# Optimization experiments

Hardware: AMD Instinct MI355X
Metric: run time of the kernel (lower is better)

Reference implementation:

```python
import jax, jax.numpy as jnp
import numpy as np

T, C, H, D = 4096, 1024, 16, 64

def setup_inputs() -> dict:
    key = jax.random.key(0)
    ks = jax.random.split(key, 6)
    s = 0.02
    return {
        "tokens": jax.random.normal(ks[0], (T, C), jnp.float32),
        "Wq": jax.random.normal(ks[1], (H, C, D), jnp.float32) * s,
        "Wk": jax.random.normal(ks[2], (H, C, D), jnp.float32) * s,
        "Wv": jax.random.normal(ks[3], (H, C, D), jnp.float32) * s,
        "Wp": jax.random.normal(ks[4], (H * D, C), jnp.float32) * s,
        "bp": jnp.zeros((C,), jnp.float32),
    }

def reference(tokens, Wq, Wk, Wv, Wp, bp):
    # per-head projections: [H, T, D]
    q = jnp.einsum("tc,hcd->htd", tokens, Wq)
    k = jnp.einsum("tc,hcd->htd", tokens, Wk)
    v = jnp.einsum("tc,hcd->htd", tokens, Wv)
    # attention scores [H, T, T], causal mask, stable softmax
    wei = jnp.einsum("htd,hsd->hts", q, k) / jnp.sqrt(jnp.float32(D))
    causal = jnp.tril(jnp.ones((T, T), dtype=bool))
    wei = jnp.where(causal, wei, -jnp.inf)
    wei = jax.nn.softmax(wei, axis=-1)
    attn = jnp.einsum("hts,hsd->htd", wei, v)
    # concat heads -> [T, H*D] (head-major order matches torch-style concat)
    out = attn.transpose(1, 0, 2).reshape(T, H * D)
    return out @ Wp + bp
```

## Files before the change

kernel.cpp:

```cpp
#include <hip/hip_runtime.h>
#include <hip/hip_bf16.h>
#include <stdint.h>

#define T_DIM 4096
#define C_DIM 1024
#define HD    1024

typedef unsigned short u16;

using bf16x8 = __attribute__((ext_vector_type(8))) short;
using bf16x4 = __attribute__((ext_vector_type(4))) short;
using f32x4  = __attribute__((ext_vector_type(4))) float;

#define MFMA16(a, b, c) __builtin_amdgcn_mfma_f32_16x16x32_bf16(a, b, c, 0, 0, 0)

#define ALPHA 0.18033688011112042f

__device__ __forceinline__ u16 f2bf(float f) {
  union { __hip_bfloat16 h; u16 u; } cv;
  cv.h = __float2bfloat16(f);
  return cv.u;
}

__device__ __forceinline__ void load_lds16(const u16* g, u16* l) {
  __builtin_amdgcn_global_load_lds(
      (const __attribute__((address_space(1))) unsigned int*)g,
      (__attribute__((address_space(3))) unsigned int*)l, 16, 0, 0);
}


__global__ void k_pack(const float* __restrict__ tokens,
                       const float* __restrict__ Wq, const float* __restrict__ Wk,
                       const float* __restrict__ Wv, const float* __restrict__ Wp,
                       u16* __restrict__ tok_b, u16* __restrict__ Wt, u16* __restrict__ Wpt) {
  __shared__ float Tsm[64][65];
  int bx = blockIdx.x;
  int t = threadIdx.x;
  if (bx < 4096) {
    int i = (bx * 256 + t) * 4;
    float4 v = *(const float4*)(tokens + i);
    bf16x4 o = { (short)f2bf(v.x), (short)f2bf(v.y), (short)f2bf(v.z), (short)f2bf(v.w) };
    *(bf16x4*)(tok_b + i) = o;
    return;
  }
  if (bx < 4864) {
    int b = bx - 4096;
    int qkv = b >> 8;
    int h = (b >> 4) & 15;
    int c0 = (b & 15) << 6;
    const float* W = (qkv == 0) ? Wq : ((qkv == 1) ? Wk : Wv);
    const float* src = W + (size_t)h * 65536 + (size_t)c0 * 64;
#pragma unroll
    for (int i = 0; i < 4; ++i) {
      int fl = i * 256 + t;
      int r = fl >> 4, c4 = fl & 15;
      float4 v = *(const float4*)(src + r * 64 + c4 * 4);
      Tsm[r][c4 * 4 + 0] = v.x; Tsm[r][c4 * 4 + 1] = v.y;
      Tsm[r][c4 * 4 + 2] = v.z; Tsm[r][c4 * 4 + 3] = v.w;
    }
    __syncthreads();
    int d = t >> 2, seg = t & 3;
    bf16x8 o0, o1;
#pragma unroll
    for (int j = 0; j < 8; ++j) o0[j] = (short)f2bf(Tsm[seg * 16 + j][d]);
#pragma unroll
    for (int j = 0; j < 8; ++j) o1[j] = (short)f2bf(Tsm[seg * 16 + 8 + j][d]);
    u16* dst = Wt + (size_t)(qkv * 1024 + h * 64 + d) * 1024 + c0 + seg * 16;
    *(bf16x8*)dst = o0;
    *(bf16x8*)(dst + 8) = o1;
    return;
  }
  {
    int b = bx - 4864;
    int k0 = (b >> 4) << 6;
    int co0 = (b & 15) << 6;
#pragma unroll
    for (int i = 0; i < 4; ++i) {
      int fl = i * 256 + t;
      int r = fl >> 4, c4 = fl & 15;
      float4 v = *(const float4*)(Wp + (size_t)(k0 + r) * 1024 + co0 + c4 * 4);
      Tsm[r][c4 * 4 + 0] = v.x; Tsm[r][c4 * 4 + 1] = v.y;
      Tsm[r][c4 * 4 + 2] = v.z; Tsm[r][c4 * 4 + 3] = v.w;
    }
    __syncthreads();
    int d = t >> 2, seg = t & 3;
    bf16x8 o0, o1;
#pragma unroll
    for (int j = 0; j < 8; ++j) o0[j] = (short)f2bf(Tsm[seg * 16 + j][d]);
#pragma unroll
    for (int j = 0; j < 8; ++j) o1[j] = (short)f2bf(Tsm[seg * 16 + 8 + j][d]);
    u16* dst = Wpt + (size_t)(co0 + d) * 1024 + k0 + seg * 16;
    *(bf16x8*)dst = o0;
    *(bf16x8*)(dst + 8) = o1;
  }
}


template<int MODE>
__global__ __launch_bounds__(256, 2) void k_gemm(
    const u16* __restrict__ A, const u16* __restrict__ B, int K,
    u16* __restrict__ Qb, u16* __restrict__ Kb, u16* __restrict__ Vt,
    float* __restrict__ Cout, const float* __restrict__ bias)
{
  __shared__ u16 Asm[2][128 * 32];
  __shared__ u16 Bsm[2][128 * 32];
  const int tid = threadIdx.x;
  const int lane = tid & 63, wid = tid >> 6;
  const int g = lane >> 4, lq = lane & 15;

  int flat = blockIdx.y * gridDim.x + blockIdx.x;
  int nwg = gridDim.x * gridDim.y;
  int sw = (flat & 7) * (nwg >> 3) + (flat >> 3);
  const int m0 = (sw / gridDim.x) * 128, n0 = (sw % gridDim.x) * 128;
  const int wm = wid >> 1, wn = wid & 1;

  const f32x4 z4 = {0.f, 0.f, 0.f, 0.f};
  f32x4 acc[4][4];
#pragma unroll
  for (int m = 0; m < 4; ++m)
#pragma unroll
    for (int n = 0; n < 4; ++n) acc[m][n] = z4;

  auto stage = [&](int k0, int buf) {
#pragma unroll
    for (int i = 0; i < 2; ++i) {
      int ch = i * 256 + tid;
      int r = ch >> 2, cp = ch & 3, cd = cp ^ ((r >> 1) & 3);
      load_lds16(A + (size_t)(m0 + r) * K + k0 + cd * 8, &Asm[buf][ch * 8]);
      load_lds16(B + (size_t)(n0 + r) * K + k0 + cd * 8, &Bsm[buf][ch * 8]);
    }
  };

  stage(0, 0);
  const int nk = K >> 5;
  const int sx = (lq >> 1) & 3;
  for (int it = 0; it < nk; ++it) {
    const int buf = it & 1;
    if (it + 1 < nk) {
      stage((it + 1) << 5, buf ^ 1);
      asm volatile("s_waitcnt vmcnt(4)" ::: "memory");
    } else {
      asm volatile("s_waitcnt vmcnt(0)" ::: "memory");
    }
    __builtin_amdgcn_s_barrier();

    bf16x8 af[4], bfr[4];
#pragma unroll
    for (int m = 0; m < 4; ++m)
      af[m] = *(const bf16x8*)&Asm[buf][(wm * 64 + m * 16 + lq) * 32 + ((g ^ sx) << 3)];
#pragma unroll
    for (int n = 0; n < 4; ++n)
      bfr[n] = *(const bf16x8*)&Bsm[buf][(wn * 64 + n * 16 + lq) * 32 + ((g ^ sx) << 3)];
#pragma unroll
    for (int m = 0; m < 4; ++m)
#pragma unroll
      for (int n = 0; n < 4; ++n)
        acc[m][n] = MFMA16(af[m], bfr[n], acc[m][n]);

    asm volatile("s_waitcnt lgkmcnt(0)" ::: "memory");
    __builtin_amdgcn_s_barrier();
  }

  if (MODE == 0) {
    const int region = n0 >> 10;
#pragma unroll
    for (int m = 0; m < 4; ++m) {
      int t0 = m0 + wm * 64 + m * 16 + 4 * g;
#pragma unroll
      for (int n = 0; n < 4; ++n) {
        int j = n0 + wn * 64 + n * 16 + lq;
        if (region == 0) {
#pragma unroll
          for (int r = 0; r < 4; ++r)
            Qb[(size_t)(t0 + r) * HD + j] = f2bf(acc[m][n][r] * ALPHA);
        } else if (region == 1) {
#pragma unroll
          for (int r = 0; r < 4; ++r) Kb[(size_t)(t0 + r) * HD + (j - 1024)] = f2bf(acc[m][n][r]);
        } else {
          bf16x4 pv = { (short)f2bf(acc[m][n][0]), (short)f2bf(acc[m][n][1]),
                        (short)f2bf(acc[m][n][2]), (short)f2bf(acc[m][n][3]) };
          *(bf16x4*)&Vt[(size_t)(j - 2048) * T_DIM + t0] = pv;
        }
      }
    }
  } else {
#pragma unroll
    for (int m = 0; m < 4; ++m) {
      int t0 = m0 + wm * 64 + m * 16 + 4 * g;
#pragma unroll
      for (int n = 0; n < 4; ++n) {
        int j = n0 + wn * 64 + n * 16 + lq;
        float bv = bias[j];
#pragma unroll
        for (int r = 0; r < 4; ++r)
          Cout[(size_t)(t0 + r) * C_DIM + j] = acc[m][n][r] + bv;
      }
    }
  }
}


#define SLOTS_PER_H 80

__global__ __launch_bounds__(256, 4) void k_attn(
    const u16* __restrict__ Qb, const u16* __restrict__ Kb,
    const u16* __restrict__ Vt, u16* __restrict__ Ob,
    float* __restrict__ PU, float* __restrict__ Pl)
{
  __shared__ u16 Ksm[2][64 * 64];
  __shared__ u16 Vsm[2][64 * 64];
  const int tid = threadIdx.x;
  const int lane = tid & 63, w = tid >> 6;
  const int g = lane >> 4, lq = lane & 15;

  int bx = blockIdx.x;
  int x = bx & 7, idx = bx >> 3;
  const int h = x * 2 + (idx & 1);
  int rem = idx >> 1;
  const int qi = rem & 31;
  const int c = rem >> 5;
  const int a = qi >> 3;
  if (c > a) return;
  const int slot = h * SLOTS_PER_H + qi + 4 * a * (a - 1) + a * (qi & 7) + c;

  const int Q0 = qi << 7;
  const int qwave = Q0 + w * 32;
  const int nt_total = (qi + 1) * 2;
  const int st = c << 4;
  const int et = min(nt_total, st + 16);

  bf16x8 qf[2][2];
#pragma unroll
  for (int qs = 0; qs < 2; ++qs) {
    const u16* qp = Qb + (size_t)(qwave + qs * 16 + lq) * HD + h * 64;
    qf[qs][0] = *(const bf16x8*)(qp + g * 8);
    qf[qs][1] = *(const bf16x8*)(qp + 32 + g * 8);
  }
  bf16x8 ones8;
#pragma unroll
  for (int j = 0; j < 8; ++j) ones8[j] = (short)0x3F80;

  const f32x4 z4 = {0.f, 0.f, 0.f, 0.f};
  f32x4 accO[2][4];
  f32x4 accL[2];
#pragma unroll
  for (int qs = 0; qs < 2; ++qs) {
    accL[qs] = z4;
#pragma unroll
    for (int n = 0; n < 4; ++n) accO[qs][n] = z4;
  }

  auto stage = [&](int kvs, int buf) {
#pragma unroll
    for (int i = 0; i < 2; ++i) {
      int ch = i * 256 + tid;
      int r = ch >> 3, cp = ch & 7, cd = cp ^ (r & 7);
      load_lds16(Kb + (size_t)(kvs + r) * HD + h * 64 + cd * 8, &Ksm[buf][ch * 8]);
    }
#pragma unroll
    for (int i = 0; i < 2; ++i) {
      int ch = i * 256 + tid;
      int r = ch >> 3, cp = ch & 7, cd = cp ^ (r & 7);
      load_lds16(Vt + (size_t)(h * 64 + r) * T_DIM + kvs + cd * 8, &Vsm[buf][ch * 8]);
    }
  };

  stage(st << 6, 0);

  for (int it = st; it < et; ++it) {
    const int kv0 = it << 6;
    const int buf = it & 1;
    if (it + 1 < et) {
      stage((it + 1) << 6, buf ^ 1);
      asm volatile("s_waitcnt vmcnt(4)" ::: "memory");
    } else {
      asm volatile("s_waitcnt vmcnt(0)" ::: "memory");
    }
    __builtin_amdgcn_s_barrier();

    if (kv0 <= qwave + 31) {
      f32x4 s[2][4];
#pragma unroll
      for (int ks = 0; ks < 4; ++ks) {
        const int kvl = ks * 16 + lq;
        const u16* kr = &Ksm[buf][kvl * 64];
        bf16x8 kf0 = *(const bf16x8*)(kr + ((g ^ (kvl & 7)) << 3));
        bf16x8 kf1 = *(const bf16x8*)(kr + (((4 + g) ^ (kvl & 7)) << 3));
        s[0][ks] = MFMA16(kf0, qf[0][0], z4);
        s[0][ks] = MFMA16(kf1, qf[0][1], s[0][ks]);
        s[1][ks] = MFMA16(kf0, qf[1][0], z4);
        s[1][ks] = MFMA16(kf1, qf[1][1], s[1][ks]);
      }

      if (kv0 + 63 > qwave) {
#pragma unroll
        for (int qs = 0; qs < 2; ++qs) {
          int qa = qwave + qs * 16 + lq;
#pragma unroll
          for (int ks = 0; ks < 4; ++ks)
#pragma unroll
            for (int r = 0; r < 4; ++r) {
              int kva = kv0 + ks * 16 + 4 * g + r;
              float sv = (kva > qa) ? -1e30f : s[qs][ks][r];
              s[qs][ks][r] = __builtin_amdgcn_exp2f(sv);
            }
        }
      } else {
#pragma unroll
        for (int qs = 0; qs < 2; ++qs)
#pragma unroll
          for (int ks = 0; ks < 4; ++ks)
#pragma unroll
            for (int r = 0; r < 4; ++r)
              s[qs][ks][r] = __builtin_amdgcn_exp2f(s[qs][ks][r]);
      }

      bf16x8 pa[2][2];
#pragma unroll
      for (int qs = 0; qs < 2; ++qs) {
        pa[qs][0] = { (short)f2bf(s[qs][0][0]), (short)f2bf(s[qs][0][1]),
                      (short)f2bf(s[qs][0][2]), (short)f2bf(s[qs][0][3]),
                      (short)f2bf(s[qs][1][0]), (short)f2bf(s[qs][1][1]),
                      (short)f2bf(s[qs][1][2]), (short)f2bf(s[qs][1][3]) };
        pa[qs][1] = { (short)f2bf(s[qs][2][0]), (short)f2bf(s[qs][2][1]),
                      (short)f2bf(s[qs][2][2]), (short)f2bf(s[qs][2][3]),
                      (short)f2bf(s[qs][3][0]), (short)f2bf(s[qs][3][1]),
                      (short)f2bf(s[qs][3][2]), (short)f2bf(s[qs][3][3]) };
      }

      accL[0] = MFMA16(pa[0][0], ones8, accL[0]);
      accL[0] = MFMA16(pa[0][1], ones8, accL[0]);
      accL[1] = MFMA16(pa[1][0], ones8, accL[1]);
      accL[1] = MFMA16(pa[1][1], ones8, accL[1]);

#pragma unroll
      for (int n = 0; n < 4; ++n) {
        const int d = n * 16 + lq;
        const u16* vr = &Vsm[buf][d * 64];
        const int xo = d & 7;
        const int go = (g & 1) * 4;
        bf16x4 lo0 = *(const bf16x4*)(vr + ((((g >> 1) + 0) ^ xo) << 3) + go);
        bf16x4 hi0 = *(const bf16x4*)(vr + ((((g >> 1) + 2) ^ xo) << 3) + go);
        bf16x4 lo1 = *(const bf16x4*)(vr + ((((g >> 1) + 4) ^ xo) << 3) + go);
        bf16x4 hi1 = *(const bf16x4*)(vr + ((((g >> 1) + 6) ^ xo) << 3) + go);
        bf16x8 vf0 = __builtin_shufflevector(lo0, hi0, 0, 1, 2, 3, 4, 5, 6, 7);
        bf16x8 vf1 = __builtin_shufflevector(lo1, hi1, 0, 1, 2, 3, 4, 5, 6, 7);
        accO[0][n] = MFMA16(pa[0][0], vf0, accO[0][n]);
        accO[0][n] = MFMA16(pa[0][1], vf1, accO[0][n]);
        accO[1][n] = MFMA16(pa[1][0], vf0, accO[1][n]);
        accO[1][n] = MFMA16(pa[1][1], vf1, accO[1][n]);
      }
    }

    asm volatile("s_waitcnt lgkmcnt(0)" ::: "memory");
    __builtin_amdgcn_s_barrier();
  }

  if (a == 0) {
#pragma unroll
    for (int qs = 0; qs < 2; ++qs) {
      float inv[4];
#pragma unroll
      for (int r = 0; r < 4; ++r) inv[r] = __builtin_amdgcn_rcpf(accL[qs][r]);
      int qrow = qwave + qs * 16 + 4 * g;
#pragma unroll
      for (int n = 0; n < 4; ++n) {
        int dcol = h * 64 + n * 16 + lq;
#pragma unroll
        for (int r = 0; r < 4; ++r)
          Ob[(size_t)(qrow + r) * HD + dcol] = f2bf(accO[qs][n][r] * inv[r]);
      }
    }
  } else {
#pragma unroll
    for (int qs = 0; qs < 2; ++qs) {
      if (lq == 0) {
#pragma unroll
        for (int r = 0; r < 4; ++r)
          Pl[(size_t)slot * 128 + w * 32 + qs * 16 + 4 * g + r] = accL[qs][r];
      }
#pragma unroll
      for (int n = 0; n < 4; ++n) {
#pragma unroll
        for (int r = 0; r < 4; ++r)
          PU[(size_t)slot * 8192 + (size_t)(w * 32 + qs * 16 + 4 * g + r) * 64 + n * 16 + lq]
              = accO[qs][n][r];
      }
    }
  }
}


__global__ void k_combine(const float* __restrict__ PU, const float* __restrict__ Pl,
                          u16* __restrict__ Ob) {
  int b = blockIdx.x;
  int h = b / 24;
  int qi = 8 + (b % 24);
  int a = qi >> 3, nch = a + 1;
  int slot0 = h * SLOTS_PER_H + qi + 4 * a * (a - 1) + a * (qi & 7);
  int t = threadIdx.x;
  int r = t >> 1, half = t & 1;

  float L = 0.f;
#pragma unroll
  for (int c = 0; c < 4; ++c)
    if (c < nch) L += Pl[(size_t)(slot0 + c) * 128 + r];

  float o[32];
#pragma unroll
  for (int j = 0; j < 32; ++j) o[j] = 0.f;
#pragma unroll
  for (int c = 0; c < 4; ++c) {
    if (c < nch) {
      const float4* up = (const float4*)(PU + (size_t)(slot0 + c) * 8192 + r * 64 + half * 32);
#pragma unroll
      for (int j = 0; j < 8; ++j) {
        float4 u = up[j];
        o[4*j+0] += u.x; o[4*j+1] += u.y;
        o[4*j+2] += u.z; o[4*j+3] += u.w;
      }
    }
  }
  float inv = 1.f / L;
  bf16x8 ov[4];
#pragma unroll
  for (int j = 0; j < 32; ++j) ov[j >> 3][j & 7] = (short)f2bf(o[j] * inv);
  u16* dst = Ob + (size_t)(qi * 128 + r) * HD + h * 64 + half * 32;
#pragma unroll
  for (int v = 0; v < 4; ++v) *(bf16x8*)(dst + v * 8) = ov[v];
}


extern "C" void kernel_launch(void* const* d_in, const int* in_sizes, int n_in,
                              void* d_out, int out_size, void* d_ws, size_t ws_size,
                              hipStream_t stream) {
  const float* tokens = (const float*)d_in[0];
  const float* Wq = (const float*)d_in[1];
  const float* Wk = (const float*)d_in[2];
  const float* Wv = (const float*)d_in[3];
  const float* Wp = (const float*)d_in[4];
  const float* bp = (const float*)d_in[5];
  float* out = (float*)d_out;

  char* w = (char*)d_ws;
  u16* tok_b = (u16*)w; w += (size_t)T_DIM * C_DIM * 2;
  u16* Ob    = tok_b;
  u16* Wt    = (u16*)w; w += (size_t)3072 * C_DIM * 2;
  u16* Wpt   = (u16*)w; w += (size_t)1024 * C_DIM * 2;
  u16* Qb    = (u16*)w; w += (size_t)T_DIM * HD * 2;
  u16* Kb    = (u16*)w; w += (size_t)T_DIM * HD * 2;
  u16* Vt    = (u16*)w; w += (size_t)T_DIM * HD * 2;
  float* PU  = (float*)w; w += (size_t)16 * SLOTS_PER_H * 8192 * 4;
  float* Pl  = (float*)w; w += (size_t)16 * SLOTS_PER_H * 128 * 4;

  k_pack<<<5120, 256, 0, stream>>>(tokens, Wq, Wk, Wv, Wp, tok_b, Wt, Wpt);

  k_gemm<0><<<dim3(24, 32), 256, 0, stream>>>(tok_b, Wt, 1024, Qb, Kb, Vt, nullptr, nullptr);
  k_attn<<<2048, 256, 0, stream>>>(Qb, Kb, Vt, Ob, PU, Pl);
  k_combine<<<384, 256, 0, stream>>>(PU, Pl, Ob);
  k_gemm<1><<<dim3(8, 32), 256, 0, stream>>>(Ob, Wpt, 1024, nullptr, nullptr, nullptr, out, bp);
}
```

Measured before the change: 236.0 us.

## Triple-buffer GEMM and attention loads and compact the attention grid

```diff
diff --git a/kernel.cpp b/kernel.cpp
--- a/kernel.cpp
+++ b/kernel.cpp
@@ -97,13 +97,13 @@
 
 
 template<int MODE>
-__global__ __launch_bounds__(256, 2) void k_gemm(
+__global__ __launch_bounds__(256, 3) void k_gemm(
     const u16* __restrict__ A, const u16* __restrict__ B, int K,
     u16* __restrict__ Qb, u16* __restrict__ Kb, u16* __restrict__ Vt,
     float* __restrict__ Cout, const float* __restrict__ bias)
 {
-  __shared__ u16 Asm[2][128 * 32];
-  __shared__ u16 Bsm[2][128 * 32];
+  __shared__ u16 Asm[3][128 * 32];
+  __shared__ u16 Bsm[3][128 * 32];
   const int tid = threadIdx.x;
   const int lane = tid & 63, wid = tid >> 6;
   const int g = lane >> 4, lq = lane & 15;
@@ -131,34 +131,36 @@
     }
   };
 
+  const int nk = K >> 5;
   stage(0, 0);
-  const int nk = K >> 5;
+  stage(32, 1);
+  asm volatile("s_waitcnt vmcnt(4)" ::: "memory");
+
   const int sx = (lq >> 1) & 3;
+  int cbuf = 0;
   for (int it = 0; it < nk; ++it) {
-    const int buf = it & 1;
-    if (it + 1 < nk) {
-      stage((it + 1) << 5, buf ^ 1);
-      asm volatile("s_waitcnt vmcnt(4)" ::: "memory");
-    } else {
-      asm volatile("s_waitcnt vmcnt(0)" ::: "memory");
-    }
     __builtin_amdgcn_s_barrier();
+    if (it + 2 < nk) {
+      int sbuf = cbuf + 2; if (sbuf >= 3) sbuf -= 3;
+      stage((it + 2) << 5, sbuf);
+    }
 
     bf16x8 af[4], bfr[4];
 #pragma unroll
     for (int m = 0; m < 4; ++m)
-      af[m] = *(const bf16x8*)&Asm[buf][(wm * 64 + m * 16 + lq) * 32 + ((g ^ sx) << 3)];
+      af[m] = *(const bf16x8*)&Asm[cbuf][(wm * 64 + m * 16 + lq) * 32 + ((g ^ sx) << 3)];
 #pragma unroll
     for (int n = 0; n < 4; ++n)
-      bfr[n] = *(const bf16x8*)&Bsm[buf][(wn * 64 + n * 16 + lq) * 32 + ((g ^ sx) << 3)];
+      bfr[n] = *(const bf16x8*)&Bsm[cbuf][(wn * 64 + n * 16 + lq) * 32 + ((g ^ sx) << 3)];
 #pragma unroll
     for (int m = 0; m < 4; ++m)
 #pragma unroll
       for (int n = 0; n < 4; ++n)
         acc[m][n] = MFMA16(af[m], bfr[n], acc[m][n]);
 
-    asm volatile("s_waitcnt lgkmcnt(0)" ::: "memory");
-    __builtin_amdgcn_s_barrier();
+    if (it + 2 < nk) asm volatile("s_waitcnt vmcnt(4) lgkmcnt(0)" ::: "memory");
+    else             asm volatile("s_waitcnt vmcnt(0) lgkmcnt(0)" ::: "memory");
+    cbuf = cbuf + 1; if (cbuf == 3) cbuf = 0;
   }
 
   if (MODE == 0) {
@@ -202,32 +204,40 @@
 
 #define SLOTS_PER_H 80
 
-__global__ __launch_bounds__(256, 4) void k_attn(
+__global__ __launch_bounds__(256, 3) void k_attn(
     const u16* __restrict__ Qb, const u16* __restrict__ Kb,
     const u16* __restrict__ Vt, u16* __restrict__ Ob,
     float* __restrict__ PU, float* __restrict__ Pl)
 {
-  __shared__ u16 Ksm[2][64 * 64];
-  __shared__ u16 Vsm[2][64 * 64];
+  __shared__ u16 Ksm[3][64 * 64];
+  __shared__ u16 Vsm[3][64 * 64];
   const int tid = threadIdx.x;
   const int lane = tid & 63, w = tid >> 6;
   const int g = lane >> 4, lq = lane & 15;
 
   int bx = blockIdx.x;
-  int x = bx & 7, idx = bx >> 3;
-  const int h = x * 2 + (idx & 1);
-  int rem = idx >> 1;
-  const int qi = rem & 31;
-  const int c = rem >> 5;
+  int xcd = bx & 7, ul = bx >> 3;
+  int h, qi, c;
+  if (ul < 96) {
+    int hp = ul / 48, k = ul % 48;
+    if (k < 8)       { qi = 8 + k;               c = 0; }
+    else if (k < 24) { int j = k - 8;  qi = 16 + (j >> 1); c = j & 1; }
+    else             { int j = k - 24; qi = 24 + j / 3;    c = j % 3; }
+    h = xcd * 2 + hp;
+  } else {
+    int v = ul - 96;
+    int hp = v >> 5, k = v & 31;
+    int m = 7 - (k >> 2), band = k & 3;
+    qi = band * 8 + m; c = band;
+    h = xcd * 2 + hp;
+  }
   const int a = qi >> 3;
-  if (c > a) return;
   const int slot = h * SLOTS_PER_H + qi + 4 * a * (a - 1) + a * (qi & 7) + c;
 
   const int Q0 = qi << 7;
   const int qwave = Q0 + w * 32;
-  const int nt_total = (qi + 1) * 2;
   const int st = c << 4;
-  const int et = min(nt_total, st + 16);
+  const int et = min((qi + 1) * 2, st + 16);
 
   bf16x8 qf[2][2];
 #pragma unroll
@@ -266,24 +276,24 @@
   };
 
   stage(st << 6, 0);
-
+  stage((st + 1) << 6, 1);
+  asm volatile("s_waitcnt vmcnt(4)" ::: "memory");
+
+  int cbuf = 0;
   for (int it = st; it < et; ++it) {
+    __builtin_amdgcn_s_barrier();
+    if (it + 2 < et) {
+      int sbuf = cbuf + 2; if (sbuf >= 3) sbuf -= 3;
+      stage((it + 2) << 6, sbuf);
+    }
+
     const int kv0 = it << 6;
-    const int buf = it & 1;
-    if (it + 1 < et) {
-      stage((it + 1) << 6, buf ^ 1);
-      asm volatile("s_waitcnt vmcnt(4)" ::: "memory");
-    } else {
-      asm volatile("s_waitcnt vmcnt(0)" ::: "memory");
-    }
-    __builtin_amdgcn_s_barrier();
-
     if (kv0 <= qwave + 31) {
       f32x4 s[2][4];
 #pragma unroll
       for (int ks = 0; ks < 4; ++ks) {
         const int kvl = ks * 16 + lq;
-        const u16* kr = &Ksm[buf][kvl * 64];
+        const u16* kr = &Ksm[cbuf][kvl * 64];
         bf16x8 kf0 = *(const bf16x8*)(kr + ((g ^ (kvl & 7)) << 3));
         bf16x8 kf1 = *(const bf16x8*)(kr + (((4 + g) ^ (kvl & 7)) << 3));
         s[0][ks] = MFMA16(kf0, qf[0][0], z4);
@@ -336,7 +346,7 @@
 #pragma unroll
       for (int n = 0; n < 4; ++n) {
         const int d = n * 16 + lq;
-        const u16* vr = &Vsm[buf][d * 64];
+        const u16* vr = &Vsm[cbuf][d * 64];
         const int xo = d & 7;
         const int go = (g & 1) * 4;
         bf16x4 lo0 = *(const bf16x4*)(vr + ((((g >> 1) + 0) ^ xo) << 3) + go);
@@ -352,8 +362,9 @@
       }
     }
 
-    asm volatile("s_waitcnt lgkmcnt(0)" ::: "memory");
-    __builtin_amdgcn_s_barrier();
+    if (it + 2 < et) asm volatile("s_waitcnt vmcnt(4) lgkmcnt(0)" ::: "memory");
+    else             asm volatile("s_waitcnt vmcnt(0) lgkmcnt(0)" ::: "memory");
+    cbuf = cbuf + 1; if (cbuf == 3) cbuf = 0;
   }
 
   if (a == 0) {
@@ -456,7 +467,7 @@
   k_pack<<<5120, 256, 0, stream>>>(tokens, Wq, Wk, Wv, Wp, tok_b, Wt, Wpt);
 
   k_gemm<0><<<dim3(24, 32), 256, 0, stream>>>(tok_b, Wt, 1024, Qb, Kb, Vt, nullptr, nullptr);
-  k_attn<<<2048, 256, 0, stream>>>(Qb, Kb, Vt, Ob, PU, Pl);
+  k_attn<<<1280, 256, 0, stream>>>(Qb, Kb, Vt, Ob, PU, Pl);
   k_combine<<<384, 256, 0, stream>>>(PU, Pl, Ob);
   k_gemm<1><<<dim3(8, 32), 256, 0, stream>>>(Ob, Wpt, 1024, nullptr, nullptr, nullptr, out, bp);
 }
```

New measurement: 206.8 us. 1.14x faster.
